# Optimization experiments

Measured on AMD Instinct MI355X. Metric: run time of the kernel, lower is better.

## Reference

```python
import jax, jax.numpy as jnp
import numpy as np

B, S, E, H = 2, 2048, 1024, 16
D = E // H  # head dim = 64

def setup_inputs() -> dict:
    key = jax.random.key(0)
    ks = jax.random.split(key, 7)
    mk = lambda k, shape, scale=1.0: (jax.random.normal(k, shape, dtype=jnp.float32) * scale)
    return {
        "query": mk(ks[0], (B, S, E)),
        "key": mk(ks[1], (B, S, E)),
        "value": mk(ks[2], (B, S, E)),
        "Wq": mk(ks[3], (E, E), 1.0 / np.sqrt(E)),
        "Wk": mk(ks[4], (E, E), 1.0 / np.sqrt(E)),
        "Wv": mk(ks[5], (E, E), 1.0 / np.sqrt(E)),
        "Wo": mk(ks[6], (E, E), 1.0 / np.sqrt(E)),
    }

def reference(query, key, value, Wq, Wk, Wv, Wo):
    # nn.Linear(bias=False): y = x @ W.T
    def split_heads(x):
        return x.reshape(B, -1, H, D).transpose(0, 2, 1, 3)  # [B,H,S,D]
    q = split_heads(query @ Wq.T)
    k = split_heads(key @ Wk.T)
    v = split_heads(value @ Wv.T)
    scores = jnp.einsum("bhqd,bhkd->bhqk", q, k) / jnp.sqrt(jnp.float32(D))
    attn = jax.nn.softmax(scores, axis=-1)  # dropout p=0 -> identity
    out = jnp.einsum("bhqk,bhkd->bhqd", attn, v)
    out = out.transpose(0, 2, 1, 3).reshape(B, -1, E)
    out = out @ Wo.T
    return out
```

## Files before the change

### kernel.cpp

```cpp
#include <hip/hip_runtime.h>
#include <stdint.h>

#define S_LEN 2048
#define HDIM  64
#define EMB   1024
#define NTOK  4096

typedef short bf16x8 __attribute__((ext_vector_type(8)));
typedef float f32x4  __attribute__((ext_vector_type(4)));

__device__ __forceinline__ unsigned short f32_bf16(float f) {
  union { float f; uint32_t u; } v; v.f = f;
  return (unsigned short)((v.u + 0x7fffu + ((v.u >> 16) & 1u)) >> 16);
}

__device__ __forceinline__ uint32_t fbits(float f) {
  union { float f; uint32_t u; } v; v.f = f; return v.u;
}

__device__ __forceinline__ uint32_t pack_bf16_trunc(float lo, float hi) {
  return __builtin_amdgcn_perm(fbits(hi), fbits(lo), 0x07060302u);
}

__device__ __forceinline__ uint32_t pack_bf16_rne(float lo, float hi) {
  return (uint32_t)f32_bf16(lo) | ((uint32_t)f32_bf16(hi) << 16);
}

__device__ __forceinline__ void async_ld16(const unsigned short* g, unsigned short* l) {
  __builtin_amdgcn_global_load_lds(
      (__attribute__((address_space(1))) unsigned int*)(uintptr_t)g,
      (__attribute__((address_space(3))) unsigned int*)l, 16, 0, 0);
}

#define CL2 0.18033688f

__global__ void cast_all(const float* __restrict__ q, const float* __restrict__ k,
                         const float* __restrict__ v, const float* __restrict__ Wq,
                         const float* __restrict__ Wk, const float* __restrict__ Wv,
                         const float* __restrict__ Wo,
                         unsigned short* __restrict__ qb, unsigned short* __restrict__ kb,
                         unsigned short* __restrict__ vb, unsigned short* __restrict__ wqb,
                         unsigned short* __restrict__ wkb, unsigned short* __restrict__ wvb,
                         unsigned short* __restrict__ wob) {
  const int b = blockIdx.x;
  const float* src; unsigned short* dst; int base;
  float scl = 1.0f;
  if (b < 12288) {
    const int which = b >> 12; base = b & 4095;
    src = which == 0 ? q : which == 1 ? k : v;
    dst = which == 0 ? qb : which == 1 ? kb : vb;
  } else {
    const int bb = b - 12288, which = bb >> 10; base = bb & 1023;
    src = which == 0 ? Wq : which == 1 ? Wk : which == 2 ? Wv : Wo;
    dst = which == 0 ? wqb : which == 1 ? wkb : which == 2 ? wvb : wob;
    if (which == 0) scl = CL2;
  }
  const int i = base * 256 + threadIdx.x;
  float4 f = ((const float4*)src)[i];
  ushort4 o;
  o.x = f32_bf16(f.x * scl); o.y = f32_bf16(f.y * scl);
  o.z = f32_bf16(f.z * scl); o.w = f32_bf16(f.w * scl);
  ((ushort4*)dst)[i] = o;
}

__global__ __launch_bounds__(256)
void gemm_qkv(const unsigned short* __restrict__ qb, const unsigned short* __restrict__ kb,
              const unsigned short* __restrict__ vb, const unsigned short* __restrict__ wqb,
              const unsigned short* __restrict__ wkb, const unsigned short* __restrict__ wvb,
              unsigned short* __restrict__ Qh, unsigned short* __restrict__ Kh,
              unsigned short* __restrict__ Vt) {
  __shared__ __align__(16) unsigned short As[2 * 128 * 32];
  __shared__ __align__(16) unsigned short Bs[2 * 128 * 32];

  const int z  = blockIdx.z;
  const int bx = blockIdx.y;
  const int by = blockIdx.x;
  const unsigned short* Xp = z == 0 ? qb  : z == 1 ? kb  : vb;
  const unsigned short* Wp = z == 0 ? wqb : z == 1 ? wkb : wvb;

  const unsigned short *A, *B;
  int tileM, tileN;
  if (z < 2) { A = Wp; tileM = bx * 128; B = Xp; tileN = by * 128; }
  else       { A = Xp; tileM = by * 128; B = Wp; tileN = bx * 128; }

  const int tid  = threadIdx.x;
  const int lane = tid & 63;
  const int wave = tid >> 6;
  const int wm = (wave >> 1) * 64;
  const int wn = (wave & 1) * 64;
  const int ccol = lane & 15;
  const int cgrp = lane >> 4;
  const int rchunk = lane >> 2;
  const int coff   = (lane & 3) * 8;

  f32x4 acc[4][4];
#pragma unroll
  for (int i = 0; i < 4; ++i)
#pragma unroll
    for (int j = 0; j < 4; ++j) acc[i][j] = 0.f;

  for (int k0 = 0; k0 < EMB; k0 += 64) {
#pragma unroll
    for (int kk = 0; kk < 2; ++kk)
#pragma unroll
      for (int i = 0; i < 2; ++i) {
        const int c = wave * 2 + i;
        const int row = c * 16 + rchunk;
        async_ld16(A + (size_t)(tileM + row) * EMB + k0 + kk * 32 + coff,
                   As + kk * 4096 + c * 512);
        async_ld16(B + (size_t)(tileN + row) * EMB + k0 + kk * 32 + coff,
                   Bs + kk * 4096 + c * 512);
      }
    __syncthreads();
#pragma unroll
    for (int kk = 0; kk < 2; ++kk) {
      bf16x8 af[4], bfm[4];
#pragma unroll
      for (int i = 0; i < 4; ++i) {
        af[i]  = *(const bf16x8*)(As + kk * 4096 + (wm + i * 16 + ccol) * 32 + cgrp * 8);
        bfm[i] = *(const bf16x8*)(Bs + kk * 4096 + (wn + i * 16 + ccol) * 32 + cgrp * 8);
      }
#pragma unroll
      for (int i = 0; i < 4; ++i)
#pragma unroll
        for (int j = 0; j < 4; ++j)
          acc[i][j] = __builtin_amdgcn_mfma_f32_16x16x32_bf16(af[i], bfm[j], acc[i][j], 0, 0, 0);
    }
    __syncthreads();
  }

  if (z < 2) {
    unsigned short* Oh = (z == 0) ? Qh : Kh;
#pragma unroll
    for (int i = 0; i < 4; ++i) {
      const int gd = tileM + wm + i * 16 + cgrp * 4;
      const int h = gd >> 6, dd = gd & 63;
#pragma unroll
      for (int j = 0; j < 4; ++j) {
        const int gt = tileN + wn + j * 16 + ccol;
        const int b = gt >> 11, s = gt & 2047;
        const uint32_t u0 = pack_bf16_rne(acc[i][j][0], acc[i][j][1]);
        const uint32_t u1 = pack_bf16_rne(acc[i][j][2], acc[i][j][3]);
        *(int2*)&Oh[((size_t)((b * 16 + h) * 2048 + s)) * 64 + dd] =
            make_int2((int)u0, (int)u1);
      }
    }
  } else {
#pragma unroll
    for (int i = 0; i < 4; ++i) {
      const int gt = tileM + wm + i * 16 + cgrp * 4;
      const int b = gt >> 11, s = gt & 2047;
#pragma unroll
      for (int j = 0; j < 4; ++j) {
        const int gd = tileN + wn + j * 16 + ccol;
        const int h = gd >> 6, dd = gd & 63;
        const uint32_t u0 = pack_bf16_rne(acc[i][j][0], acc[i][j][1]);
        const uint32_t u1 = pack_bf16_rne(acc[i][j][2], acc[i][j][3]);
        *(int2*)&Vt[((size_t)((b * 16 + h) * 64 + dd)) * 2048 + s] =
            make_int2((int)u0, (int)u1);
      }
    }
  }
}

__global__ __launch_bounds__(256)
void gemm_out(const unsigned short* __restrict__ Ctx, const unsigned short* __restrict__ Wo,
              float* __restrict__ Out) {
  __shared__ __align__(16) unsigned short As[2 * 64 * 32];
  __shared__ __align__(16) unsigned short Bs[2 * 128 * 32];

  const int tid  = threadIdx.x;
  const int lane = tid & 63;
  const int wave = tid >> 6;
  const int wm = (wave >> 1) * 32;
  const int wn = (wave & 1) * 64;
  const int ccol = lane & 15;
  const int cgrp = lane >> 4;
  const int rchunk = lane >> 2;
  const int coff   = (lane & 3) * 8;
  const int tileM = blockIdx.y * 64;
  const int tileN = blockIdx.x * 128;

  f32x4 acc[2][4];
#pragma unroll
  for (int i = 0; i < 2; ++i)
#pragma unroll
    for (int j = 0; j < 4; ++j) acc[i][j] = 0.f;

  for (int k0 = 0; k0 < EMB; k0 += 64) {
#pragma unroll
    for (int kk = 0; kk < 2; ++kk) {
      {
        const int row = wave * 16 + rchunk;
        async_ld16(Wo + (size_t)(tileM + row) * EMB + k0 + kk * 32 + coff,
                   As + kk * 2048 + wave * 512);
      }
#pragma unroll
      for (int i = 0; i < 2; ++i) {
        const int c = wave * 2 + i;
        const int row = c * 16 + rchunk;
        async_ld16(Ctx + (size_t)(tileN + row) * EMB + k0 + kk * 32 + coff,
                   Bs + kk * 4096 + c * 512);
      }
    }
    __syncthreads();
#pragma unroll
    for (int kk = 0; kk < 2; ++kk) {
      bf16x8 af[2], bfm[4];
#pragma unroll
      for (int i = 0; i < 2; ++i)
        af[i] = *(const bf16x8*)(As + kk * 2048 + (wm + i * 16 + ccol) * 32 + cgrp * 8);
#pragma unroll
      for (int j = 0; j < 4; ++j)
        bfm[j] = *(const bf16x8*)(Bs + kk * 4096 + (wn + j * 16 + ccol) * 32 + cgrp * 8);
#pragma unroll
      for (int i = 0; i < 2; ++i)
#pragma unroll
        for (int j = 0; j < 4; ++j)
          acc[i][j] = __builtin_amdgcn_mfma_f32_16x16x32_bf16(af[i], bfm[j], acc[i][j], 0, 0, 0);
    }
    __syncthreads();
  }

#pragma unroll
  for (int i = 0; i < 2; ++i) {
    const int odim = tileM + wm + i * 16 + cgrp * 4;
#pragma unroll
    for (int j = 0; j < 4; ++j) {
      const int gt = tileN + wn + j * 16 + ccol;
      float4 o = make_float4(acc[i][j][0], acc[i][j][1], acc[i][j][2], acc[i][j][3]);
      *(float4*)&Out[(size_t)gt * 1024 + odim] = o;
    }
  }
}

__global__ __launch_bounds__(256, 2)
void attn_kernel(const unsigned short* __restrict__ Qh,
                 const unsigned short* __restrict__ Kh,
                 const unsigned short* __restrict__ Vt,
                 unsigned short* __restrict__ Ctx) {
  __shared__ __align__(16) unsigned short Ks[2 * 64 * 64];
  __shared__ __align__(16) unsigned short Vs[2 * 64 * 64];
  __shared__ __align__(16) unsigned short Ps[128 * 64];

  const int tid  = threadIdx.x;
  const int lane = tid & 63;
  const int wave = tid >> 6;
  const int bh = blockIdx.x;
  const int q0 = blockIdx.y * 128;
  const unsigned short* Qg = Qh + ((size_t)bh * S_LEN + q0) * HDIM;
  const unsigned short* Kg = Kh + (size_t)bh * S_LEN * HDIM;
  const unsigned short* Vg = Vt + (size_t)bh * HDIM * S_LEN;

  const int ccol = lane & 15;
  const int cgrp = lane >> 4;
  const int mrow = wave * 32;
  const int sw7  = ccol & 7;

#pragma unroll
  for (int i = 0; i < 4; ++i) {
    const int cid = i * 256 + tid;
    const int row = cid >> 3, j = cid & 7, g = j ^ (row & 7);
    *(int4*)&Ps[row * 64 + j * 8] = *(const int4*)&Qg[(size_t)row * 64 + g * 8];
  }
  __syncthreads();
  bf16x8 aq[2][2];
#pragma unroll
  for (int g = 0; g < 2; ++g)
#pragma unroll
    for (int kk = 0; kk < 2; ++kk) {
      const int pp = (kk * 4 + cgrp) ^ sw7;
      aq[g][kk] = *(const bf16x8*)&Ps[(mrow + g * 16 + ccol) * 64 + pp * 8];
    }
  unsigned short* Pw = Ps + wave * 2048;

  const int r0 = tid >> 3, j0 = tid & 7;
  const int r1 = r0 + 32;
  const int sA = j0 ^ (r0 & 7);
  const int sB = j0 ^ (r1 & 7);

  int4 kr0 = *(const int4*)&Kg[(size_t)r0 * 64 + sA * 8];
  int4 kr1 = *(const int4*)&Kg[(size_t)r1 * 64 + sB * 8];
  int4 vr0 = *(const int4*)&Vg[(size_t)r0 * 2048 + sA * 8];
  int4 vr1 = *(const int4*)&Vg[(size_t)r1 * 2048 + sB * 8];

  f32x4 l4[2];
  l4[0] = 0.f; l4[1] = 0.f;
  f32x4 o_acc[4][2];
#pragma unroll
  for (int dt = 0; dt < 4; ++dt) { o_acc[dt][0] = 0.f; o_acc[dt][1] = 0.f; }

  for (int i = 0; i < 32; ++i) {
    unsigned short* Kb = Ks + (i & 1) * 4096;
    unsigned short* Vb = Vs + (i & 1) * 4096;
    *(int4*)&Kb[r0 * 64 + j0 * 8] = kr0;
    *(int4*)&Kb[r1 * 64 + j0 * 8] = kr1;
    *(int4*)&Vb[r0 * 64 + j0 * 8] = vr0;
    *(int4*)&Vb[r1 * 64 + j0 * 8] = vr1;
    __syncthreads();
    if (i < 31) {
      const int nb = (i + 1) * 64;
      kr0 = *(const int4*)&Kg[(size_t)(nb + r0) * 64 + sA * 8];
      kr1 = *(const int4*)&Kg[(size_t)(nb + r1) * 64 + sB * 8];
      vr0 = *(const int4*)&Vg[(size_t)r0 * 2048 + nb + sA * 8];
      vr1 = *(const int4*)&Vg[(size_t)r1 * 2048 + nb + sB * 8];
    }

    f32x4 sc[2][4];
#pragma unroll
    for (int nt = 0; nt < 4; ++nt) {
      const int krow = nt * 16 + ccol;
      bf16x8 ak0 = *(const bf16x8*)&Kb[krow * 64 + ((cgrp) ^ sw7) * 8];
      bf16x8 ak1 = *(const bf16x8*)&Kb[krow * 64 + ((4 + cgrp) ^ sw7) * 8];
#pragma unroll
      for (int g = 0; g < 2; ++g) {
        f32x4 s = 0.f;
        s = __builtin_amdgcn_mfma_f32_16x16x32_bf16(ak0, aq[g][0], s, 0, 0, 0);
        s = __builtin_amdgcn_mfma_f32_16x16x32_bf16(ak1, aq[g][1], s, 0, 0, 0);
        sc[g][nt] = s;
      }
    }

#pragma unroll
    for (int g = 0; g < 2; ++g)
#pragma unroll
      for (int nt = 0; nt < 4; ++nt) {
#pragma unroll
        for (int r = 0; r < 4; ++r)
          sc[g][nt][r] = __builtin_amdgcn_exp2f(sc[g][nt][r]);
        l4[g] += sc[g][nt];
      }

#pragma unroll
    for (int g = 0; g < 2; ++g) {
      unsigned short* Pr = Pw + (g * 16 + ccol) * 64;
#pragma unroll
      for (int nt = 0; nt < 4; ++nt) {
        const uint32_t u0 = pack_bf16_trunc(sc[g][nt][0], sc[g][nt][1]);
        const uint32_t u1 = pack_bf16_trunc(sc[g][nt][2], sc[g][nt][3]);
        const int pp = (nt * 2 + (cgrp >> 1)) ^ sw7;
        *(int2*)&Pr[pp * 8 + (cgrp & 1) * 4] = make_int2((int)u0, (int)u1);
      }
    }
    asm volatile("s_waitcnt lgkmcnt(0)" ::: "memory");
    bf16x8 ap[2][2];
#pragma unroll
    for (int g = 0; g < 2; ++g)
#pragma unroll
      for (int kk = 0; kk < 2; ++kk) {
        const int pp = (kk * 4 + cgrp) ^ sw7;
        ap[g][kk] = *(const bf16x8*)&Pw[(g * 16 + ccol) * 64 + pp * 8];
      }

#pragma unroll
    for (int dt = 0; dt < 4; ++dt) {
      const int vrow = dt * 16 + ccol;
      bf16x8 av0 = *(const bf16x8*)&Vb[vrow * 64 + ((cgrp) ^ sw7) * 8];
      bf16x8 av1 = *(const bf16x8*)&Vb[vrow * 64 + ((4 + cgrp) ^ sw7) * 8];
#pragma unroll
      for (int g = 0; g < 2; ++g) {
        f32x4 o = o_acc[dt][g];
        o = __builtin_amdgcn_mfma_f32_16x16x32_bf16(av0, ap[g][0], o, 0, 0, 0);
        o = __builtin_amdgcn_mfma_f32_16x16x32_bf16(av1, ap[g][1], o, 0, 0, 0);
        o_acc[dt][g] = o;
      }
    }
  }

  const int b = bh >> 4, h = bh & 15;
#pragma unroll
  for (int g = 0; g < 2; ++g) {
    float l_i = l4[g][0] + l4[g][1] + l4[g][2] + l4[g][3];
    l_i += __shfl_xor(l_i, 16);
    l_i += __shfl_xor(l_i, 32);
    const float inv_l = __builtin_amdgcn_rcpf(l_i) * 1.00195f;
    const int srow = q0 + mrow + g * 16 + ccol;
#pragma unroll
    for (int dt = 0; dt < 4; ++dt) {
      float o0 = o_acc[dt][g][0] * inv_l, o1 = o_acc[dt][g][1] * inv_l;
      float o2 = o_acc[dt][g][2] * inv_l, o3 = o_acc[dt][g][3] * inv_l;
      uint32_t u0 = pack_bf16_rne(o0, o1);
      uint32_t u1 = pack_bf16_rne(o2, o3);
      const int col = h * 64 + dt * 16 + cgrp * 4;
      *(int2*)&Ctx[((size_t)(b * 2048 + srow)) * 1024 + col] = make_int2((int)u0, (int)u1);
    }
  }
}

extern "C" void kernel_launch(void* const* d_in, const int* in_sizes, int n_in,
                              void* d_out, int out_size, void* d_ws, size_t ws_size,
                              hipStream_t stream) {
  const float* q  = (const float*)d_in[0];
  const float* k  = (const float*)d_in[1];
  const float* v  = (const float*)d_in[2];
  const float* Wq = (const float*)d_in[3];
  const float* Wk = (const float*)d_in[4];
  const float* Wv = (const float*)d_in[5];
  const float* Wo = (const float*)d_in[6];

  const size_t tok = (size_t)NTOK * EMB;
  const size_t wsz = (size_t)EMB * EMB;
  unsigned short* p = (unsigned short*)d_ws;
  unsigned short* qb  = p; p += tok;
  unsigned short* kb  = p; p += tok;
  unsigned short* vb  = p; p += tok;
  unsigned short* wqb = p; p += wsz;
  unsigned short* wkb = p; p += wsz;
  unsigned short* wvb = p; p += wsz;
  unsigned short* wob = p; p += wsz;
  unsigned short* Qh  = p; p += tok;
  unsigned short* Kh  = p; p += tok;
  unsigned short* Vt  = p; p += tok;
  unsigned short* Ctx = p; p += tok;

  cast_all<<<dim3(16384), dim3(256), 0, stream>>>(q, k, v, Wq, Wk, Wv, Wo,
                                                  qb, kb, vb, wqb, wkb, wvb, wob);

  gemm_qkv<<<dim3(32, 8, 3), dim3(256), 0, stream>>>(qb, kb, vb, wqb, wkb, wvb,
                                                     Qh, Kh, Vt);

  attn_kernel<<<dim3(32, 16), dim3(256), 0, stream>>>(Qh, Kh, Vt, Ctx);

  gemm_out<<<dim3(32, 16), dim3(256), 0, stream>>>(Ctx, wob, (float*)d_out);
}
```

Before: 212.5 us.

## Redistribute softmax probabilities via permlane swaps instead of LDS round-trip

```diff
diff --git a/kernel.cpp b/kernel.cpp
--- a/kernel.cpp
+++ b/kernel.cpp
@@ -8,6 +8,8 @@
 
 typedef short bf16x8 __attribute__((ext_vector_type(8)));
 typedef float f32x4  __attribute__((ext_vector_type(4)));
+typedef uint32_t u32x4 __attribute__((ext_vector_type(4)));
+typedef uint32_t u32x2 __attribute__((ext_vector_type(2)));
 
 __device__ __forceinline__ unsigned short f32_bf16(float f) {
   union { float f; uint32_t u; } v; v.f = f;
@@ -30,6 +32,18 @@
   __builtin_amdgcn_global_load_lds(
       (__attribute__((address_space(1))) unsigned int*)(uintptr_t)g,
       (__attribute__((address_space(3))) unsigned int*)l, 16, 0, 0);
+}
+
+__device__ __forceinline__ void p_swap(uint32_t& x, uint32_t& y) {
+  u32x2 r1 = __builtin_amdgcn_permlane32_swap(x, y, false, false);
+  uint32_t a = r1[0], b = r1[1];
+#if __has_builtin(__builtin_amdgcn_permlane16_swap)
+  u32x2 r2 = __builtin_amdgcn_permlane16_swap(a, b, false, false);
+  x = r2[0]; y = r2[1];
+#else
+  asm volatile("v_permlane16_swap_b32 %0, %1" : "+v"(a), "+v"(b));
+  x = a; y = b;
+#endif
 }
 
 #define CL2 0.18033688f
@@ -272,7 +286,6 @@
       const int pp = (kk * 4 + cgrp) ^ sw7;
       aq[g][kk] = *(const bf16x8*)&Ps[(mrow + g * 16 + ccol) * 64 + pp * 8];
     }
-  unsigned short* Pw = Ps + wave * 2048;
 
   const int r0 = tid >> 3, j0 = tid & 7;
   const int r1 = r0 + 32;
@@ -307,6 +320,7 @@
     }
 
     f32x4 sc[2][4];
+    __builtin_amdgcn_s_setprio(1);
 #pragma unroll
     for (int nt = 0; nt < 4; ++nt) {
       const int krow = nt * 16 + ccol;
@@ -320,6 +334,7 @@
         sc[g][nt] = s;
       }
     }
+    __builtin_amdgcn_s_setprio(0);
 
 #pragma unroll
     for (int g = 0; g < 2; ++g)
@@ -331,27 +346,34 @@
         l4[g] += sc[g][nt];
       }
 
+    bf16x8 ap[2][2];
 #pragma unroll
     for (int g = 0; g < 2; ++g) {
-      unsigned short* Pr = Pw + (g * 16 + ccol) * 64;
+      uint32_t u[4][2];
 #pragma unroll
       for (int nt = 0; nt < 4; ++nt) {
-        const uint32_t u0 = pack_bf16_trunc(sc[g][nt][0], sc[g][nt][1]);
-        const uint32_t u1 = pack_bf16_trunc(sc[g][nt][2], sc[g][nt][3]);
-        const int pp = (nt * 2 + (cgrp >> 1)) ^ sw7;
-        *(int2*)&Pr[pp * 8 + (cgrp & 1) * 4] = make_int2((int)u0, (int)u1);
-      }
-    }
-    asm volatile("s_waitcnt lgkmcnt(0)" ::: "memory");
-    bf16x8 ap[2][2];
-#pragma unroll
-    for (int g = 0; g < 2; ++g)
+        u[nt][0] = pack_bf16_trunc(sc[g][nt][0], sc[g][nt][1]);
+        u[nt][1] = pack_bf16_trunc(sc[g][nt][2], sc[g][nt][3]);
+      }
+      uint32_t w[2][4];
+#pragma unroll
+      for (int kk = 0; kk < 2; ++kk)
+#pragma unroll
+        for (int h = 0; h < 2; ++h) {
+          uint32_t x = u[2 * kk][h], y = u[2 * kk + 1][h];
+          p_swap(x, y);
+          w[kk][h] = x; w[kk][2 + h] = y;
+        }
 #pragma unroll
       for (int kk = 0; kk < 2; ++kk) {
-        const int pp = (kk * 4 + cgrp) ^ sw7;
-        ap[g][kk] = *(const bf16x8*)&Pw[(g * 16 + ccol) * 64 + pp * 8];
-      }
-
+        union { u32x4 u; bf16x8 b; } cv;
+        cv.u[0] = w[kk][0]; cv.u[1] = w[kk][1];
+        cv.u[2] = w[kk][2]; cv.u[3] = w[kk][3];
+        ap[g][kk] = cv.b;
+      }
+    }
+
+    __builtin_amdgcn_s_setprio(1);
 #pragma unroll
     for (int dt = 0; dt < 4; ++dt) {
       const int vrow = dt * 16 + ccol;
@@ -365,6 +387,7 @@
         o_acc[dt][g] = o;
       }
     }
+    __builtin_amdgcn_s_setprio(0);
   }
 
   const int b = bh >> 4, h = bh & 15;
```

Result: faster. 205.6 us (-3.3%).
